# Performance work log

Hardware: AMD Instinct MI355X
Metric: run time of the kernel (lower is better)

The kernel has to match this reference:

```python
import jax, jax.numpy as jnp
import numpy as np

B, Cin, Cout, H, W = 4, 256, 256, 64, 64
DG, KH, KW = 2, 3, 3        # deformable_groups=2, kernel 3x3
K = KH * KW
CG = Cin // DG


def setup_inputs() -> dict:
    key = jax.random.key(0)
    ks = jax.random.split(key, 4)
    x = jax.random.normal(ks[0], (B, Cin, H, W), jnp.float32)
    # offset/mask-predicting 3x3 conv: 3*DG*K = 54 output channels
    # (small weights so sampled offsets stay in a realistic +-few-pixel range)
    w_off = jax.random.normal(ks[1], (3 * DG * K, Cin, KH, KW), jnp.float32) * 0.01
    b_off = jnp.zeros((3 * DG * K,), jnp.float32)
    weight = jax.random.normal(ks[2], (Cout, Cin, KH, KW), jnp.float32) * (1.0 / np.sqrt(Cin * K))
    bias = jnp.zeros((Cout,), jnp.float32)
    return {"x": x, "w_off": w_off, "b_off": b_off, "weight": weight, "bias": bias}


def _dcn_forward(x, w_off, b_off, weight, bias):
    # 1) predict offsets + modulation mask with a regular 3x3 conv
    om = jax.lax.conv_general_dilated(
        x, w_off, window_strides=(1, 1), padding=((1, 1), (1, 1)),
        dimension_numbers=('NCHW', 'OIHW', 'NCHW'))
    om = om + b_off[None, :, None, None]
    off = om[:, :2 * DG * K].reshape(B, DG, 2, K, H, W)        # [.,.,(dy,dx),k,h,w]
    mask = jax.nn.sigmoid(om[:, 2 * DG * K:]).reshape(B, DG, K, H, W)

    # 2) sampling positions: base grid (stride 1, pad 1, dilation 1) + learned offsets
    ky = jnp.repeat(jnp.arange(KH), KW).astype(jnp.float32)    # [K]
    kx = jnp.tile(jnp.arange(KW), KH).astype(jnp.float32)
    gy = jnp.arange(H, dtype=jnp.float32)
    gx = jnp.arange(W, dtype=jnp.float32)
    py = off[:, :, 0] + (gy[None, None, None, :, None] + ky[None, None, :, None, None] - 1.0)  # [B,DG,K,H,W]
    px = off[:, :, 1] + (gx[None, None, None, None, :] + kx[None, None, :, None, None] - 1.0)

    y0 = jnp.floor(py); x0 = jnp.floor(px)
    wy1 = py - y0; wx1 = px - x0
    wy0 = 1.0 - wy1; wx0 = 1.0 - wx1
    y0i = y0.astype(jnp.int32); x0i = x0.astype(jnp.int32)

    imgf = x.reshape(B, DG, CG, H * W)  # channel groups share their group's offsets

    def gather(iy, ix):
        # zero padding outside the image, as in the DCNv2 CUDA kernel
        valid = ((iy >= 0) & (iy < H) & (ix >= 0) & (ix < W)).astype(x.dtype)  # [B,DG,K,H,W]
        idx = jnp.clip(iy, 0, H - 1) * W + jnp.clip(ix, 0, W - 1)
        idx = idx.reshape(B, DG, K * H * W)
        v = jax.vmap(jax.vmap(lambda im, ii: im[:, ii]))(imgf, idx)  # [B,DG,CG,K*H*W]
        return v.reshape(B, DG, CG, K, H, W) * valid[:, :, None]

    # 3) bilinear interpolation of the 4 corners
    sampled = (gather(y0i,     x0i)     * (wy0 * wx0)[:, :, None]
             + gather(y0i,     x0i + 1) * (wy0 * wx1)[:, :, None]
             + gather(y0i + 1, x0i)     * (wy1 * wx0)[:, :, None]
             + gather(y0i + 1, x0i + 1) * (wy1 * wx1)[:, :, None])
    sampled = sampled * mask[:, :, None]  # modulation (DCNv2)

    # 4) weighted accumulation == grouped contraction over (channel, tap)
    wr = weight.reshape(Cout, DG, CG, K)
    out = jnp.einsum('odck,bdckhw->bohw', wr, sampled) + bias[None, :, None, None]
    return out


def reference(x, w_off, b_off, weight, bias):
    return _dcn_forward(x, w_off, b_off, weight, bias)
```

## Files before the change

### kernel.cpp

```cpp
#include <hip/hip_runtime.h>
#include <cstdint>

#define HW 4096

typedef __attribute__((ext_vector_type(8))) short bf16x8;
typedef __attribute__((ext_vector_type(4))) float f32x4;

__device__ __forceinline__ short f2bf(float f) {
    union { float f; uint32_t u; } v; v.f = f;
    uint32_t u = v.u;
    uint32_t r = (u + 0x7FFFu + ((u >> 16) & 1u)) >> 16;
    return (short)(r & 0xFFFFu);
}
__device__ __forceinline__ uint32_t cvtpk(float lo, float hi) {
    uint32_t r;
    asm("v_cvt_pk_bf16_f32 %0, %1, %2" : "=v"(r) : "v"(lo), "v"(hi));
    return r;
}
__device__ __forceinline__ float blo(uint32_t u) { return __uint_as_float(u << 16); }
__device__ __forceinline__ float bhi(uint32_t u) { return __uint_as_float(u & 0xFFFF0000u); }

__global__ __launch_bounds__(256) void k_pre(
    const float* __restrict__ x, const float* __restrict__ weight,
    const float* __restrict__ w_off, unsigned short* __restrict__ xT,
    short* __restrict__ a2r, short* __restrict__ wTb2)
{
    const int bid = blockIdx.x;
    if (bid < 1024) {
        __shared__ unsigned short s[64][65];
        const int t = threadIdx.x, lane = t & 63, grp = t >> 6;
        const int hw0 = (bid & 63) * 64, c0 = ((bid >> 6) & 3) * 64, b = bid >> 8;
#pragma unroll
        for (int j = 0; j < 16; ++j) {
            int cc = grp * 16 + j;
            float v = x[((size_t)(b * 256 + c0 + cc)) * HW + hw0 + lane];
            s[cc][lane] = (unsigned short)f2bf(v);
        }
        __syncthreads();
#pragma unroll
        for (int j = 0; j < 16; ++j) {
            int hw2 = grp * 16 + j;
            xT[((size_t)b * HW + hw0 + hw2) * 256 + c0 + lane] = s[lane][hw2];
        }
    } else {
        int e = (bid - 1024) * 256 + threadIdx.x;
        if (e < 589824) {
            int el = e & 7;
            int lane = (e >> 3) & 63;
            int rg = (e >> 9) & 15;
            int ss = (e >> 13) & 3;
            int j = e >> 15;
            int o = rg * 16 + (lane & 15);
            int cch = ss * 32 + (lane >> 4) * 8 + el;
            int dg = j / 9, tap = j - dg * 9;
            a2r[e] = f2bf(weight[o * 2304 + (dg * 128 + cch) * 9 + tap]);
        } else {
            int e2 = e - 589824;
            int el = e2 & 7;
            int lane = (e2 >> 3) & 63;
            int mi2 = (e2 >> 9) & 3;
            int c = e2 >> 11;
            int o = mi2 * 16 + (lane & 15);
            int k = c * 32 + ((lane >> 4) << 3) + el;
            int tap = k >> 8, ch = k & 255;
            wTb2[e2] = (o < 54) ? f2bf(w_off[(o * 256 + ch) * 9 + tap]) : (short)0;
        }
    }
}

__global__ __launch_bounds__(512, 4) void k_fused(
    const short* __restrict__ A2r, const short* __restrict__ wTb2,
    const unsigned short* __restrict__ xT, const float* __restrict__ b_off,
    const float* __restrict__ bias, float* __restrict__ out)
{
    __shared__ short Bs[2][4][32 * 32];
    __shared__ float omS[64][32];
    __shared__ float4 PlnW[18][32];
    __shared__ int4   PlnI[18][32];
    const int t = threadIdx.x;
    const int wid = __builtin_amdgcn_readfirstlane(t >> 6);
    const int lane = t & 63;
    const int quad = lane >> 4, l16 = lane & 15;
    const int wr = wid;

    const int lin = blockIdx.x;
    const int bn = ((lin & 7) << 6) | (lin >> 3);

    const int n0 = bn * 32, b = n0 >> 12;
    const unsigned short* xb16 = xT + (size_t)b * HW * 256;
    const char* xbb = (const char*)xb16;
    const int px = t >> 4;
    const int cc = (t >> 2) & 3;
    const int q8 = (t & 3) * 8;

    const int qo  = t >> 7;
    const int px2 = (t >> 2) & 31;
    const int ksh2 = (t & 3) * 8;
    const int nn2 = n0 + px2;
    const int ph = (nn2 & 4095) >> 6, pw_ = nn2 & 63;
    const int bsw2 = ((t & 3) ^ ((px2 >> 1) & 3)) * 8;
    const int mi2 = wid & 3, ni2 = wid >> 2;
    const short* AwOm = wTb2 + mi2 * 512 + lane * 8;

    f32x4 accOm = (f32x4){0.f, 0.f, 0.f, 0.f};
    uint4 arOm[4];
    uint4 gv;

    auto omload = [&](int gi) -> uint4 {
        const int c = gi * 4 + qo;
        const int tap = c >> 3, c0 = (c & 7) * 32;
        const int hh = ph + tap / 3 - 1, ww = pw_ + tap % 3 - 1;
        uint4 bv = {0u, 0u, 0u, 0u};
        if (hh >= 0 && hh < 64 && ww >= 0 && ww < 64)
            bv = *(const uint4*)(xb16 + (size_t)(hh * 64 + ww) * 256 + c0 + ksh2);
        return bv;
    };
    auto aloadOm = [&](int gi) {
#pragma unroll
        for (int q = 0; q < 4; ++q)
            arOm[q] = *(const uint4*)(AwOm + (size_t)(gi * 4 + q) * 2048);
    };

    gv = omload(0);
    *(uint4*)&Bs[0][qo][px2 * 32 + bsw2] = gv;
    aloadOm(0);

#pragma unroll 2
    for (int gi = 0; gi < 18; ++gi) {
        const int p = gi & 1;
        __syncthreads();
        if (gi + 1 < 18) gv = omload(gi + 1);
        __builtin_amdgcn_sched_barrier(0);
#pragma unroll
        for (int q = 0; q < 4; ++q) {
            const int row = ni2 * 16 + l16;
            bf16x8 bq = *(const bf16x8*)&Bs[p][q][row * 32 + (quad ^ ((row >> 1) & 3)) * 8];
            accOm = __builtin_amdgcn_mfma_f32_16x16x32_bf16(
                *(const bf16x8*)&arOm[q], bq, accOm, 0, 0, 0);
        }
        if (gi + 1 < 18) {
            *(uint4*)&Bs[1 - p][qo][px2 * 32 + bsw2] = gv;
            aloadOm(gi + 1);
        }
    }
    __syncthreads();
    {
        const int mrow = mi2 * 16 + (lane >> 4) * 4;
        const int pcol = ni2 * 16 + l16;
#pragma unroll
        for (int rr = 0; rr < 4; ++rr)
            omS[mrow + rr][pcol] = accOm[rr];
    }
    __syncthreads();

    for (int s = wid; s < 18; s += 8) {
        if (lane < 32) {
            const int nn = n0 + lane;
            const int dg = s >= 9 ? 1 : 0, tap = s - dg * 9;
            const int hh = (nn >> 6) & 63, ww2 = nn & 63;
            const int cdy = dg * 18 + tap, cdx = cdy + 9, cms = 36 + dg * 9 + tap;
            float dy = b_off[cdy] + omS[cdy][lane];
            float dx = b_off[cdx] + omS[cdx][lane];
            float ms = b_off[cms] + omS[cms][lane];
            ms = 1.f / (1.f + __expf(-ms));
            float py = dy + (float)(hh + tap / 3 - 1);
            float qx = dx + (float)(ww2 + tap % 3 - 1);
            float y0f = floorf(py), x0f = floorf(qx);
            float wy1 = py - y0f, wx1 = qx - x0f;
            float wy0 = 1.f - wy1, wx0 = 1.f - wx1;
            int y0 = (int)y0f, x0 = (int)x0f;
            int y1 = y0 + 1, x1 = x0 + 1;
            bool vy0 = (y0 >= 0) & (y0 < 64), vy1 = (y1 >= 0) & (y1 < 64);
            bool vx0 = (x0 >= 0) & (x0 < 64), vx1 = (x1 >= 0) & (x1 < 64);
            int cy0 = min(max(y0, 0), 63), cy1 = min(max(y1, 0), 63);
            int cx0 = min(max(x0, 0), 63), cx1 = min(max(x1, 0), 63);
            float4 wv;
            wv.x = (vy0 && vx0) ? wy0 * wx0 * ms : 0.f;
            wv.y = (vy0 && vx1) ? wy0 * wx1 * ms : 0.f;
            wv.z = (vy1 && vx0) ? wy1 * wx0 * ms : 0.f;
            wv.w = (vy1 && vx1) ? wy1 * wx1 * ms : 0.f;
            int4 iv = make_int4((cy0 * 64 + cx0) << 9, (cy0 * 64 + cx1) << 9,
                                (cy1 * 64 + cx0) << 9, (cy1 * 64 + cx1) << 9);
            PlnW[s][lane] = wv;
            PlnI[s][lane] = iv;
        }
    }
    __syncthreads();

    const short* Aw = A2r + (size_t)(wr * 2) * 512 + lane * 8;

    f32x4 acc[2][2];
#pragma unroll
    for (int i = 0; i < 2; ++i)
#pragma unroll
        for (int j = 0; j < 2; ++j) acc[i][j] = (f32x4){0.f, 0.f, 0.f, 0.f};

    float4 pw[2];
    int4 pi[2];
    uint4 g[4];
    uint4 ar[8];

    auto pwload = [&](int S) { pw[S & 1] = PlnW[S][px]; };
    auto piload = [&](int S) { pi[S & 1] = PlnI[S][px]; };
    auto gather = [&](int j) {
        const int cb = ((j >= 9 ? 128 : 0) + cc * 32 + q8) * 2;
        const int4 i4 = pi[j & 1];
        g[0] = *(const uint4*)(xbb + i4.x + cb);
        g[1] = *(const uint4*)(xbb + i4.y + cb);
        g[2] = *(const uint4*)(xbb + i4.z + cb);
        g[3] = *(const uint4*)(xbb + i4.w + cb);
    };
    auto aload = [&](int j) {
#pragma unroll
        for (int ss = 0; ss < 4; ++ss)
#pragma unroll
            for (int mi = 0; mi < 2; ++mi)
                ar[ss * 2 + mi] =
                    *(const uint4*)(Aw + (size_t)(j * 4 + ss) * 8192 + mi * 512);
    };
    const int bsw = ((t & 3) ^ ((px >> 1) & 3)) * 8;
    auto packwrite = [&](int j, int buf) {
        const float4 w4 = pw[j & 1];
        float a0 = w4.x * blo(g[0].x) + w4.y * blo(g[1].x) + w4.z * blo(g[2].x) + w4.w * blo(g[3].x);
        float a1 = w4.x * bhi(g[0].x) + w4.y * bhi(g[1].x) + w4.z * bhi(g[2].x) + w4.w * bhi(g[3].x);
        float a2v = w4.x * blo(g[0].y) + w4.y * blo(g[1].y) + w4.z * blo(g[2].y) + w4.w * blo(g[3].y);
        float a3 = w4.x * bhi(g[0].y) + w4.y * bhi(g[1].y) + w4.z * bhi(g[2].y) + w4.w * bhi(g[3].y);
        float a4 = w4.x * blo(g[0].z) + w4.y * blo(g[1].z) + w4.z * blo(g[2].z) + w4.w * blo(g[3].z);
        float a5 = w4.x * bhi(g[0].z) + w4.y * bhi(g[1].z) + w4.z * bhi(g[2].z) + w4.w * bhi(g[3].z);
        float a6 = w4.x * blo(g[0].w) + w4.y * blo(g[1].w) + w4.z * blo(g[2].w) + w4.w * blo(g[3].w);
        float a7 = w4.x * bhi(g[0].w) + w4.y * bhi(g[1].w) + w4.z * bhi(g[2].w) + w4.w * bhi(g[3].w);
        uint4 o;
        o.x = cvtpk(a0, a1); o.y = cvtpk(a2v, a3);
        o.z = cvtpk(a4, a5); o.w = cvtpk(a6, a7);
        *(uint4*)&Bs[buf][cc][px * 32 + bsw] = o;
    };
    auto mfmaPhase = [&](int p) {
#pragma unroll
        for (int ss = 0; ss < 4; ++ss) {
            bf16x8 bfr[2];
#pragma unroll
            for (int ni = 0; ni < 2; ++ni) {
                const int row = ni * 16 + l16;
                bfr[ni] = *(const bf16x8*)&Bs[p][ss][row * 32 + (quad ^ ((row >> 1) & 3)) * 8];
            }
#pragma unroll
            for (int mi = 0; mi < 2; ++mi) {
                bf16x8 af = *(const bf16x8*)&ar[ss * 2 + mi];
#pragma unroll
                for (int ni = 0; ni < 2; ++ni)
                    acc[mi][ni] = __builtin_amdgcn_mfma_f32_16x16x32_bf16(
                        af, bfr[ni], acc[mi][ni], 0, 0, 0);
            }
        }
    };

    pwload(0);
    piload(0);
    gather(0);
    aload(0);
    packwrite(0, 0);
    pwload(1);
    piload(1);

#pragma unroll 2
    for (int i = 0; i < 18; ++i) {
        const int p = i & 1;
        __syncthreads();
        if (i + 1 < 18) gather(i + 1);
        if (i + 2 < 18) { pwload(i + 2); piload(i + 2); }
        __builtin_amdgcn_sched_barrier(0);
        mfmaPhase(p);
        if (i + 1 < 18) aload(i + 1);
        if (i + 1 < 18) packwrite(i + 1, 1 - p);
    }

    const int m0 = wr * 32;
#pragma unroll
    for (int mi = 0; mi < 2; ++mi)
#pragma unroll
        for (int ni = 0; ni < 2; ++ni) {
            int nn = n0 + ni * 16 + l16;
            int bidx = nn >> 12, hw = nn & 4095;
            float* op = out + (size_t)bidx * 256 * 4096 + hw;
#pragma unroll
            for (int r = 0; r < 4; ++r) {
                int m = m0 + mi * 16 + quad * 4 + r;
                op[(size_t)m * 4096] = acc[mi][ni][r] + bias[m];
            }
        }
}

extern "C" void kernel_launch(void* const* d_in, const int* in_sizes, int n_in,
                              void* d_out, int out_size, void* d_ws, size_t ws_size,
                              hipStream_t stream)
{
    const float* x      = (const float*)d_in[0];
    const float* w_off  = (const float*)d_in[1];
    const float* b_off  = (const float*)d_in[2];
    const float* weight = (const float*)d_in[3];
    const float* bias   = (const float*)d_in[4];
    float* out = (float*)d_out;
    char* ws = (char*)d_ws;

    unsigned short* xT   = (unsigned short*)(ws);
    short*          a2r  = (short*)(ws + 8388608);
    short*          wTb2 = (short*)(ws + 9568256);

    hipLaunchKernelGGL(k_pre, dim3(3904), dim3(256), 0, stream,
                       x, weight, w_off, xT, a2r, wTb2);
    hipLaunchKernelGGL(k_fused, dim3(512), dim3(512), 0, stream,
                       a2r, wTb2, xT, b_off, bias, out);
}
```

Measured before the change: 124.9 us.

## Merge preprocessing and fused DCN kernels via grid-wide atomic barrier

Folds the bf16 transpose of x and the weight repacking into the main kernel, so each of the 512 blocks handles a slice of the preprocessing and then waits at a global atomic-counter barrier before running the fused offset-conv and deformable GEMM. This removes a kernel launch and the gap between the two kernels, at the cost of a memset and a spin barrier that needs all blocks to be resident at once. It also stages the offset-conv weight tiles into LDS with global_load_lds and double buffering, prefetching the x tile two steps ahead instead of loading weights into registers.

```diff
diff --git a/kernel.cpp b/kernel.cpp
--- a/kernel.cpp
+++ b/kernel.cpp
@@ -2,6 +2,7 @@
 #include <cstdint>
 
 #define HW 4096
+#define NBLK 512
 
 typedef __attribute__((ext_vector_type(8))) short bf16x8;
 typedef __attribute__((ext_vector_type(4))) float f32x4;
@@ -19,128 +20,148 @@
 }
 __device__ __forceinline__ float blo(uint32_t u) { return __uint_as_float(u << 16); }
 __device__ __forceinline__ float bhi(uint32_t u) { return __uint_as_float(u & 0xFFFF0000u); }
-
-__global__ __launch_bounds__(256) void k_pre(
+__device__ __forceinline__ void glds16(const void* g, void* l) {
+    __builtin_amdgcn_global_load_lds(
+        (const __attribute__((address_space(1))) void*)g,
+        (__attribute__((address_space(3))) void*)l, 16, 0, 0);
+}
+
+__global__ __launch_bounds__(512, 4) void k_all(
     const float* __restrict__ x, const float* __restrict__ weight,
-    const float* __restrict__ w_off, unsigned short* __restrict__ xT,
-    short* __restrict__ a2r, short* __restrict__ wTb2)
-{
-    const int bid = blockIdx.x;
-    if (bid < 1024) {
-        __shared__ unsigned short s[64][65];
-        const int t = threadIdx.x, lane = t & 63, grp = t >> 6;
-        const int hw0 = (bid & 63) * 64, c0 = ((bid >> 6) & 3) * 64, b = bid >> 8;
-#pragma unroll
-        for (int j = 0; j < 16; ++j) {
-            int cc = grp * 16 + j;
-            float v = x[((size_t)(b * 256 + c0 + cc)) * HW + hw0 + lane];
-            s[cc][lane] = (unsigned short)f2bf(v);
-        }
-        __syncthreads();
-#pragma unroll
-        for (int j = 0; j < 16; ++j) {
-            int hw2 = grp * 16 + j;
-            xT[((size_t)b * HW + hw0 + hw2) * 256 + c0 + lane] = s[lane][hw2];
-        }
-    } else {
-        int e = (bid - 1024) * 256 + threadIdx.x;
-        if (e < 589824) {
-            int el = e & 7;
-            int lane = (e >> 3) & 63;
-            int rg = (e >> 9) & 15;
-            int ss = (e >> 13) & 3;
-            int j = e >> 15;
-            int o = rg * 16 + (lane & 15);
-            int cch = ss * 32 + (lane >> 4) * 8 + el;
-            int dg = j / 9, tap = j - dg * 9;
-            a2r[e] = f2bf(weight[o * 2304 + (dg * 128 + cch) * 9 + tap]);
-        } else {
-            int e2 = e - 589824;
-            int el = e2 & 7;
-            int lane = (e2 >> 3) & 63;
-            int mi2 = (e2 >> 9) & 3;
-            int c = e2 >> 11;
-            int o = mi2 * 16 + (lane & 15);
-            int k = c * 32 + ((lane >> 4) << 3) + el;
-            int tap = k >> 8, ch = k & 255;
-            wTb2[e2] = (o < 54) ? f2bf(w_off[(o * 256 + ch) * 9 + tap]) : (short)0;
-        }
-    }
-}
-
-__global__ __launch_bounds__(512, 4) void k_fused(
-    const short* __restrict__ A2r, const short* __restrict__ wTb2,
-    const unsigned short* __restrict__ xT, const float* __restrict__ b_off,
-    const float* __restrict__ bias, float* __restrict__ out)
+    const float* __restrict__ w_off, const float* __restrict__ b_off,
+    const float* __restrict__ bias, unsigned short* __restrict__ xT,
+    short* __restrict__ a2r, short* __restrict__ wTb2,
+    unsigned int* __restrict__ cnt, float* __restrict__ out)
 {
     __shared__ short Bs[2][4][32 * 32];
+    __shared__ short AsOm[2][8192];
     __shared__ float omS[64][32];
     __shared__ float4 PlnW[18][32];
     __shared__ int4   PlnI[18][32];
+
     const int t = threadIdx.x;
     const int wid = __builtin_amdgcn_readfirstlane(t >> 6);
     const int lane = t & 63;
     const int quad = lane >> 4, l16 = lane & 15;
-    const int wr = wid;
-
     const int lin = blockIdx.x;
+
+    {
+        unsigned short (*trS)[65] = (unsigned short (*)[65])(&AsOm[0][0]);
+        const int grp = t >> 6, ln = t & 63;
+#pragma unroll
+        for (int k = 0; k < 2; ++k) {
+            const int tid = lin * 2 + k;
+            const int hw0 = (tid & 63) * 64, c0 = ((tid >> 6) & 3) * 64;
+            const int bb = tid >> 8;
+#pragma unroll
+            for (int j = 0; j < 8; ++j) {
+                int cc2 = grp * 8 + j;
+                trS[cc2][ln] = (unsigned short)f2bf(
+                    x[((size_t)(bb * 256 + c0 + cc2)) * HW + hw0 + ln]);
+            }
+            __syncthreads();
+#pragma unroll
+            for (int j = 0; j < 8; ++j) {
+                int hw2 = grp * 8 + j;
+                xT[((size_t)bb * HW + hw0 + hw2) * 256 + c0 + ln] = trS[ln][hw2];
+            }
+            __syncthreads();
+        }
+#pragma unroll
+        for (int q = 0; q < 3; ++q) {
+            int r = q * 512 + t;
+            if (r < 1440) {
+                int e = lin * 1440 + r;
+                if (e < 589824) {
+                    int el = e & 7;
+                    int ln2 = (e >> 3) & 63;
+                    int rg = (e >> 9) & 15;
+                    int ss = (e >> 13) & 3;
+                    int j = e >> 15;
+                    int o = rg * 16 + (ln2 & 15);
+                    int cch = ss * 32 + (ln2 >> 4) * 8 + el;
+                    int dg = j / 9, tap = j - dg * 9;
+                    a2r[e] = f2bf(weight[o * 2304 + (dg * 128 + cch) * 9 + tap]);
+                } else {
+                    int e2 = e - 589824;
+                    int el = e2 & 7;
+                    int ln2 = (e2 >> 3) & 63;
+                    int mi2w = (e2 >> 9) & 3;
+                    int c = e2 >> 11;
+                    int o = mi2w * 16 + (ln2 & 15);
+                    int k2 = c * 32 + ((ln2 >> 4) << 3) + el;
+                    int tap = k2 >> 8, ch = k2 & 255;
+                    wTb2[e2] = (o < 54) ? f2bf(w_off[(o * 256 + ch) * 9 + tap])
+                                        : (short)0;
+                }
+            }
+        }
+    }
+
+    __threadfence();
+    __syncthreads();
+    if (t == 0) {
+        __hip_atomic_fetch_add(cnt, 1u, __ATOMIC_ACQ_REL, __HIP_MEMORY_SCOPE_AGENT);
+        while (__hip_atomic_load(cnt, __ATOMIC_ACQUIRE, __HIP_MEMORY_SCOPE_AGENT)
+               < (unsigned)NBLK)
+            __builtin_amdgcn_s_sleep(8);
+    }
+    __syncthreads();
+
     const int bn = ((lin & 7) << 6) | (lin >> 3);
-
     const int n0 = bn * 32, b = n0 >> 12;
     const unsigned short* xb16 = xT + (size_t)b * HW * 256;
     const char* xbb = (const char*)xb16;
     const int px = t >> 4;
     const int cc = (t >> 2) & 3;
     const int q8 = (t & 3) * 8;
-
-    const int qo  = t >> 7;
-    const int px2 = (t >> 2) & 31;
-    const int ksh2 = (t & 3) * 8;
-    const int nn2 = n0 + px2;
-    const int ph = (nn2 & 4095) >> 6, pw_ = nn2 & 63;
-    const int bsw2 = ((t & 3) ^ ((px2 >> 1) & 3)) * 8;
+    const int ph = ((n0 + px) & 4095) >> 6, pw_ = (n0 + px) & 63;
+    const int bsw = ((t & 3) ^ ((px >> 1) & 3)) * 8;
     const int mi2 = wid & 3, ni2 = wid >> 2;
-    const short* AwOm = wTb2 + mi2 * 512 + lane * 8;
 
     f32x4 accOm = (f32x4){0.f, 0.f, 0.f, 0.f};
-    uint4 arOm[4];
-    uint4 gv;
+    uint4 bvOm[2];
 
     auto omload = [&](int gi) -> uint4 {
-        const int c = gi * 4 + qo;
+        const int c = gi * 4 + cc;
         const int tap = c >> 3, c0 = (c & 7) * 32;
         const int hh = ph + tap / 3 - 1, ww = pw_ + tap % 3 - 1;
         uint4 bv = {0u, 0u, 0u, 0u};
         if (hh >= 0 && hh < 64 && ww >= 0 && ww < 64)
-            bv = *(const uint4*)(xb16 + (size_t)(hh * 64 + ww) * 256 + c0 + ksh2);
+            bv = *(const uint4*)(xb16 + (size_t)(hh * 64 + ww) * 256 + c0 + q8);
         return bv;
     };
-    auto aloadOm = [&](int gi) {
-#pragma unroll
-        for (int q = 0; q < 4; ++q)
-            arOm[q] = *(const uint4*)(AwOm + (size_t)(gi * 4 + q) * 2048);
-    };
-
-    gv = omload(0);
-    *(uint4*)&Bs[0][qo][px2 * 32 + bsw2] = gv;
-    aloadOm(0);
+    auto stageOmA = [&](int gi, int buf) {
+#pragma unroll
+        for (int r = 0; r < 2; ++r) {
+            const int f = 2 * wid + r;
+            const int cc3 = f >> 2, mi3 = f & 3;
+            glds16(wTb2 + (size_t)(gi * 4 + cc3) * 2048 + mi3 * 512 + lane * 8,
+                   &AsOm[buf][f * 512 + lane * 8]);
+        }
+    };
+
+    stageOmA(0, 0);
+    bvOm[0] = omload(0);
+    *(uint4*)&Bs[0][cc][px * 32 + bsw] = bvOm[0];
+    bvOm[1] = omload(1);
 
 #pragma unroll 2
     for (int gi = 0; gi < 18; ++gi) {
         const int p = gi & 1;
         __syncthreads();
-        if (gi + 1 < 18) gv = omload(gi + 1);
+        if (gi < 17) {
+            stageOmA(gi + 1, 1 - p);
+            *(uint4*)&Bs[1 - p][cc][px * 32 + bsw] = bvOm[(gi + 1) & 1];
+        }
+        if (gi + 2 < 18) bvOm[gi & 1] = omload(gi + 2);
         __builtin_amdgcn_sched_barrier(0);
 #pragma unroll
         for (int q = 0; q < 4; ++q) {
             const int row = ni2 * 16 + l16;
+            bf16x8 aq = *(const bf16x8*)&AsOm[p][(q * 4 + mi2) * 512 + lane * 8];
             bf16x8 bq = *(const bf16x8*)&Bs[p][q][row * 32 + (quad ^ ((row >> 1) & 3)) * 8];
-            accOm = __builtin_amdgcn_mfma_f32_16x16x32_bf16(
-                *(const bf16x8*)&arOm[q], bq, accOm, 0, 0, 0);
-        }
-        if (gi + 1 < 18) {
-            *(uint4*)&Bs[1 - p][qo][px2 * 32 + bsw2] = gv;
-            aloadOm(gi + 1);
+            accOm = __builtin_amdgcn_mfma_f32_16x16x32_bf16(aq, bq, accOm, 0, 0, 0);
         }
     }
     __syncthreads();
@@ -187,7 +208,8 @@
     }
     __syncthreads();
 
-    const short* Aw = A2r + (size_t)(wr * 2) * 512 + lane * 8;
+    const int wr = wid;
+    const short* Aw = a2r + (size_t)(wr * 2) * 512 + lane * 8;
 
     f32x4 acc[2][2];
 #pragma unroll
@@ -218,7 +240,6 @@
                 ar[ss * 2 + mi] =
                     *(const uint4*)(Aw + (size_t)(j * 4 + ss) * 8192 + mi * 512);
     };
-    const int bsw = ((t & 3) ^ ((px >> 1) & 3)) * 8;
     auto packwrite = [&](int j, int buf) {
         const float4 w4 = pw[j & 1];
         float a0 = w4.x * blo(g[0].x) + w4.y * blo(g[1].x) + w4.z * blo(g[2].x) + w4.w * blo(g[3].x);
@@ -305,9 +326,9 @@
     unsigned short* xT   = (unsigned short*)(ws);
     short*          a2r  = (short*)(ws + 8388608);
     short*          wTb2 = (short*)(ws + 9568256);
-
-    hipLaunchKernelGGL(k_pre, dim3(3904), dim3(256), 0, stream,
-                       x, weight, w_off, xT, a2r, wTb2);
-    hipLaunchKernelGGL(k_fused, dim3(512), dim3(512), 0, stream,
-                       a2r, wTb2, xT, b_off, bias, out);
-}
+    unsigned int*   cnt  = (unsigned int*)(ws + 10485760);
+
+    hipMemsetAsync(cnt, 0, 4, stream);
+    hipLaunchKernelGGL(k_all, dim3(NBLK), dim3(512), 0, stream,
+                       x, weight, w_off, b_off, bias, xT, a2r, wTb2, cnt, out);
+}
```

Measured after the change: 230.6 us. +84.6%, slower.

## Stage offset-conv weights into LDS via direct global-to-LDS loads, deepen prefetch

Applied to the files above, without the earlier changes.

The offset/mask conv phase now copies the A-operand weight tiles into a new double-buffered LDS array using global_load_lds, instead of each wave loading its own copy into registers. The input-patch gather is prefetched two iterations ahead, and its thread mapping is changed to reuse the main-phase px/cc/q8 indices. This is meant to cut redundant global weight traffic and to hide load latency better. In exchange it uses 32KB more LDS, which may lower occupancy under the 512x4 launch bound, and adds extra LDS reads before each MFMA.

```diff
diff --git a/kernel.cpp b/kernel.cpp
--- a/kernel.cpp
+++ b/kernel.cpp
@@ -19,6 +19,11 @@
 }
 __device__ __forceinline__ float blo(uint32_t u) { return __uint_as_float(u << 16); }
 __device__ __forceinline__ float bhi(uint32_t u) { return __uint_as_float(u & 0xFFFF0000u); }
+__device__ __forceinline__ void glds16(const void* g, void* l) {
+    __builtin_amdgcn_global_load_lds(
+        (const __attribute__((address_space(1))) void*)g,
+        (__attribute__((address_space(3))) void*)l, 16, 0, 0);
+}
 
 __global__ __launch_bounds__(256) void k_pre(
     const float* __restrict__ x, const float* __restrict__ weight,
@@ -74,6 +79,7 @@
     const float* __restrict__ bias, float* __restrict__ out)
 {
     __shared__ short Bs[2][4][32 * 32];
+    __shared__ short AsOm[2][8192];
     __shared__ float omS[64][32];
     __shared__ float4 PlnW[18][32];
     __shared__ int4   PlnI[18][32];
@@ -81,7 +87,6 @@
     const int wid = __builtin_amdgcn_readfirstlane(t >> 6);
     const int lane = t & 63;
     const int quad = lane >> 4, l16 = lane & 15;
-    const int wr = wid;
 
     const int lin = blockIdx.x;
     const int bn = ((lin & 7) << 6) | (lin >> 3);
@@ -92,55 +97,53 @@
     const int px = t >> 4;
     const int cc = (t >> 2) & 3;
     const int q8 = (t & 3) * 8;
-
-    const int qo  = t >> 7;
-    const int px2 = (t >> 2) & 31;
-    const int ksh2 = (t & 3) * 8;
-    const int nn2 = n0 + px2;
-    const int ph = (nn2 & 4095) >> 6, pw_ = nn2 & 63;
-    const int bsw2 = ((t & 3) ^ ((px2 >> 1) & 3)) * 8;
+    const int ph = ((n0 + px) & 4095) >> 6, pw_ = (n0 + px) & 63;
+    const int bsw = ((t & 3) ^ ((px >> 1) & 3)) * 8;
     const int mi2 = wid & 3, ni2 = wid >> 2;
-    const short* AwOm = wTb2 + mi2 * 512 + lane * 8;
 
     f32x4 accOm = (f32x4){0.f, 0.f, 0.f, 0.f};
-    uint4 arOm[4];
-    uint4 gv;
+    uint4 bvOm[2];
 
     auto omload = [&](int gi) -> uint4 {
-        const int c = gi * 4 + qo;
+        const int c = gi * 4 + cc;
         const int tap = c >> 3, c0 = (c & 7) * 32;
         const int hh = ph + tap / 3 - 1, ww = pw_ + tap % 3 - 1;
         uint4 bv = {0u, 0u, 0u, 0u};
         if (hh >= 0 && hh < 64 && ww >= 0 && ww < 64)
-            bv = *(const uint4*)(xb16 + (size_t)(hh * 64 + ww) * 256 + c0 + ksh2);
+            bv = *(const uint4*)(xb16 + (size_t)(hh * 64 + ww) * 256 + c0 + q8);
         return bv;
     };
-    auto aloadOm = [&](int gi) {
-#pragma unroll
-        for (int q = 0; q < 4; ++q)
-            arOm[q] = *(const uint4*)(AwOm + (size_t)(gi * 4 + q) * 2048);
-    };
-
-    gv = omload(0);
-    *(uint4*)&Bs[0][qo][px2 * 32 + bsw2] = gv;
-    aloadOm(0);
+    auto stageOmA = [&](int gi, int buf) {
+#pragma unroll
+        for (int r = 0; r < 2; ++r) {
+            const int f = 2 * wid + r;
+            const int cc3 = f >> 2, mi3 = f & 3;
+            glds16(wTb2 + (size_t)(gi * 4 + cc3) * 2048 + mi3 * 512 + lane * 8,
+                   &AsOm[buf][f * 512 + lane * 8]);
+        }
+    };
+
+    stageOmA(0, 0);
+    bvOm[0] = omload(0);
+    *(uint4*)&Bs[0][cc][px * 32 + bsw] = bvOm[0];
+    bvOm[1] = omload(1);
 
 #pragma unroll 2
     for (int gi = 0; gi < 18; ++gi) {
         const int p = gi & 1;
         __syncthreads();
-        if (gi + 1 < 18) gv = omload(gi + 1);
+        if (gi < 17) {
+            stageOmA(gi + 1, 1 - p);
+            *(uint4*)&Bs[1 - p][cc][px * 32 + bsw] = bvOm[(gi + 1) & 1];
+        }
+        if (gi + 2 < 18) bvOm[gi & 1] = omload(gi + 2);
         __builtin_amdgcn_sched_barrier(0);
 #pragma unroll
         for (int q = 0; q < 4; ++q) {
             const int row = ni2 * 16 + l16;
+            bf16x8 aq = *(const bf16x8*)&AsOm[p][(q * 4 + mi2) * 512 + lane * 8];
             bf16x8 bq = *(const bf16x8*)&Bs[p][q][row * 32 + (quad ^ ((row >> 1) & 3)) * 8];
-            accOm = __builtin_amdgcn_mfma_f32_16x16x32_bf16(
-                *(const bf16x8*)&arOm[q], bq, accOm, 0, 0, 0);
-        }
-        if (gi + 1 < 18) {
-            *(uint4*)&Bs[1 - p][qo][px2 * 32 + bsw2] = gv;
-            aloadOm(gi + 1);
+            accOm = __builtin_amdgcn_mfma_f32_16x16x32_bf16(aq, bq, accOm, 0, 0, 0);
         }
     }
     __syncthreads();
@@ -187,6 +190,7 @@
     }
     __syncthreads();
 
+    const int wr = wid;
     const short* Aw = A2r + (size_t)(wr * 2) * 512 + lane * 8;
 
     f32x4 acc[2][2];
@@ -218,7 +222,6 @@
                 ar[ss * 2 + mi] =
                     *(const uint4*)(Aw + (size_t)(j * 4 + ss) * 8192 + mi * 512);
     };
-    const int bsw = ((t & 3) ^ ((px >> 1) & 3)) * 8;
     auto packwrite = [&](int j, int buf) {
         const float4 w4 = pw[j & 1];
         float a0 = w4.x * blo(g[0].x) + w4.y * blo(g[1].x) + w4.z * blo(g[2].x) + w4.w * blo(g[3].x);
```

Result: slower. 127.5 us (+2.1%).
